# Optimization experiments

Measured on AMD Instinct MI355X. Metric: run time of the kernel, lower is better.

Reference implementation:

```python
import jax, jax.numpy as jnp
import numpy as np

NHEAD = 16
EPS = 1e-5

def layer_norm(x, g, b):
    mu = jnp.mean(x, axis=-1, keepdims=True)
    var = jnp.mean(jnp.square(x - mu), axis=-1, keepdims=True)
    return (x - mu) * jax.lax.rsqrt(var + EPS) * g + b

def setup_inputs() -> dict:
    key = jax.random.key(0)
    ks = jax.random.split(key, 12)
    d_model, d_hid = 1024, 4096  # MHA num_hiddens == dim_feedforward (source quirk)
    B, S = 2, 2048
    s_in = 1.0 / np.sqrt(d_model)
    s_hid = 1.0 / np.sqrt(d_hid)
    return {
        "x": jax.random.normal(ks[0], (B, S, d_model), jnp.float32),
        "Wq": jax.random.normal(ks[1], (d_model, d_hid), jnp.float32) * s_in,
        "Wk": jax.random.normal(ks[2], (d_model, d_hid), jnp.float32) * s_in,
        "Wv": jax.random.normal(ks[3], (d_model, d_hid), jnp.float32) * s_in,
        "Wo": jax.random.normal(ks[4], (d_hid, d_model), jnp.float32) * s_hid,
        "W1": jax.random.normal(ks[5], (d_model, d_hid), jnp.float32) * s_in,
        "b1": jnp.zeros((d_hid,), jnp.float32),
        "W2": jax.random.normal(ks[6], (d_hid, d_model), jnp.float32) * s_hid,
        "b2": jnp.zeros((d_model,), jnp.float32),
        "g1": jnp.ones((d_model,), jnp.float32),
        "be1": jnp.zeros((d_model,), jnp.float32),
        "g2": jnp.ones((d_model,), jnp.float32),
        "be2": jnp.zeros((d_model,), jnp.float32),
    }

def reference(x, Wq, Wk, Wv, Wo, W1, b1, W2, b2, g1, be1, g2, be2):
    B, S, D = x.shape
    H = NHEAD
    # pre-norm attention branch (dropout = identity at eval)
    x1 = layer_norm(x, g1, be1)
    q = (x1 @ Wq).reshape(B, S, H, -1)  # [B,S,H,dh], dh = num_hiddens/H
    k = (x1 @ Wk).reshape(B, S, H, -1)
    v = (x1 @ Wv).reshape(B, S, H, -1)
    dh = q.shape[-1]
    scores = jnp.einsum('bqhd,bkhd->bhqk', q, k) / jnp.sqrt(jnp.float32(dh))
    attn = jax.nn.softmax(scores, axis=-1)
    ctx = jnp.einsum('bhqk,bkhd->bqhd', attn, v).reshape(B, S, -1)
    x = x + ctx @ Wo
    # pre-norm FFN branch
    x2 = layer_norm(x, g2, be2)
    h = jax.nn.relu(x2 @ W1 + b1)
    out = x + (h @ W2 + b2)
    return out
```

## Files before the change

kernel.cpp:

```cpp
#include <hip/hip_runtime.h>
#include <hip/hip_bf16.h>
#include <stdint.h>

using bf16x8 = __attribute__((ext_vector_type(8))) __bf16;
using f32x4  = __attribute__((ext_vector_type(4))) float;

__device__ __forceinline__ uint16_t f2bf(float f) {
    uint32_t u = __builtin_bit_cast(uint32_t, f);
    u += 0x7FFFu + ((u >> 16) & 1u);
    return (uint16_t)(u >> 16);
}
__device__ __forceinline__ uint32_t pack2bf(float lo, float hi) {
    return (uint32_t)f2bf(lo) | ((uint32_t)f2bf(hi) << 16);
}

__device__ __forceinline__ void gld_lds16(const void* g, void* l) {
    __builtin_amdgcn_global_load_lds(
        (const __attribute__((address_space(1))) void*)g,
        (__attribute__((address_space(3))) void*)l,
        16, 0, 0);
}

__global__ __launch_bounds__(256)
void wconv(const float* __restrict__ in, uint16_t* __restrict__ out, int R, int C) {
    __shared__ float t[32][33];
    int c0 = blockIdx.x * 32, r0 = blockIdx.y * 32;
    int tx = threadIdx.x & 31, ty = threadIdx.x >> 5;
    #pragma unroll
    for (int i = 0; i < 32; i += 8)
        t[ty + i][tx] = in[(size_t)(r0 + ty + i) * C + c0 + tx];
    __syncthreads();
    #pragma unroll
    for (int i = 0; i < 32; i += 8)
        out[(size_t)(c0 + ty + i) * R + r0 + tx] = f2bf(t[tx][ty + i]);
}

__global__ __launch_bounds__(256)
void ln_bf16(const float* __restrict__ x, const float* __restrict__ gw,
             const float* __restrict__ bw, uint16_t* __restrict__ out) {
    const int D = 1024;
    int row = blockIdx.x;
    float4 v = ((const float4*)(x + (size_t)row * D))[threadIdx.x];
    float s  = v.x + v.y + v.z + v.w;
    float ss = v.x * v.x + v.y * v.y + v.z * v.z + v.w * v.w;
    #pragma unroll
    for (int m = 1; m < 64; m <<= 1) {
        s  += __shfl_xor(s, m);
        ss += __shfl_xor(ss, m);
    }
    __shared__ float red[8];
    int wid = threadIdx.x >> 6, lane = threadIdx.x & 63;
    if (lane == 0) { red[wid] = s; red[4 + wid] = ss; }
    __syncthreads();
    s  = red[0] + red[1] + red[2] + red[3];
    ss = red[4] + red[5] + red[6] + red[7];
    float mu  = s * (1.f / 1024.f);
    float var = ss * (1.f / 1024.f) - mu * mu;
    float rstd = rsqrtf(var + 1e-5f);
    float4 gv = ((const float4*)gw)[threadIdx.x];
    float4 bv = ((const float4*)bw)[threadIdx.x];
    ushort4 o;
    o.x = f2bf((v.x - mu) * rstd * gv.x + bv.x);
    o.y = f2bf((v.y - mu) * rstd * gv.y + bv.y);
    o.z = f2bf((v.z - mu) * rstd * gv.z + bv.z);
    o.w = f2bf((v.w - mu) * rstd * gv.w + bv.w);
    ((ushort4*)(out + (size_t)row * D))[threadIdx.x] = o;
}

template <int EPI>
__global__ __launch_bounds__(256, 2)
void gemm_bt(const uint16_t* __restrict__ A, const uint16_t* __restrict__ B,
             void* __restrict__ Cp, const float* __restrict__ bias,
             const float* __restrict__ resid, int M, int N, int K) {
    __shared__ uint16_t sA[128 * 32];
    __shared__ uint16_t sB[128 * 32];
    int bid = blockIdx.x;
    int cpx = gridDim.x >> 3;
    bid = (bid & 7) * cpx + (bid >> 3);
    int nbn  = N >> 7;
    int brow = (bid / nbn) << 7;
    int bcol = (bid % nbn) << 7;
    int t = threadIdx.x;
    int wid = t >> 6, lane = t & 63;
    int wr = (wid >> 1) << 6, wc = (wid & 1) << 6;
    int q = lane & 15, g = lane >> 4;

    f32x4 acc[4][4] = {};

    const uint16_t* Abase = A + (size_t)brow * K + ((lane & 3) << 3);
    const uint16_t* Bbase = B + (size_t)bcol * K + ((lane & 3) << 3);
    int rsub = lane >> 2;

    for (int kt = 0; kt < K; kt += 32) {
        __syncthreads();
        #pragma unroll
        for (int i = 0; i < 2; ++i) {
            int chunk = i * 4 + wid;
            int row = chunk * 16 + rsub;
            gld_lds16(Abase + (size_t)row * K + kt, &sA[chunk * 512]);
            gld_lds16(Bbase + (size_t)row * K + kt, &sB[chunk * 512]);
        }
        __syncthreads();
        bf16x8 af[4], bfr[4];
        #pragma unroll
        for (int i = 0; i < 4; ++i)
            af[i] = *(const bf16x8*)&sA[(wr + i * 16 + q) * 32 + g * 8];
        #pragma unroll
        for (int j = 0; j < 4; ++j)
            bfr[j] = *(const bf16x8*)&sB[(wc + j * 16 + q) * 32 + g * 8];
        #pragma unroll
        for (int i = 0; i < 4; ++i)
            #pragma unroll
            for (int j = 0; j < 4; ++j)
                acc[i][j] = __builtin_amdgcn_mfma_f32_16x16x32_bf16(
                    af[i], bfr[j], acc[i][j], 0, 0, 0);
    }

    float* Cf = (float*)Cp;
    #pragma unroll
    for (int i = 0; i < 4; ++i) {
        #pragma unroll
        for (int j = 0; j < 4; ++j) {
            #pragma unroll
            for (int r = 0; r < 4; ++r) {
                int gr = brow + wr + i * 16 + g * 4 + r;
                int gc = bcol + wc + j * 16 + q;
                float v = acc[i][j][r];
                size_t idx = (size_t)gr * N + gc;
                if constexpr (EPI == 2) {
                    Cf[idx] = v + bias[gc] + resid[idx];
                } else {
                    Cf[idx] = v + resid[idx];
                }
            }
        }
    }
}

template <int EPI>
__global__ __launch_bounds__(512, 2)
void gemm256(const uint16_t* __restrict__ A, const uint16_t* __restrict__ B,
             void* __restrict__ Cp, const float* __restrict__ bias,
             int M, int N, int K) {
    __shared__ uint8_t smem[131072];
    int bid = blockIdx.x;
    int cpx = gridDim.x >> 3;
    bid = (bid & 7) * cpx + (bid >> 3);
    int nbn  = N >> 8;
    int brow = (bid / nbn) << 8;
    int bcol = (bid % nbn) << 8;
    int t0 = threadIdx.x;
    int wid = t0 >> 6, lane = t0 & 63;
    int wr = wid >> 2, wc = wid & 3;
    int q = lane & 15, g = lane >> 4;

    const uint16_t* Asw = A + (size_t)(brow + (lane >> 3)) * K + (((lane & 7) ^ (lane >> 3)) << 3);
    const uint16_t* Bsw = B + (size_t)(bcol + (lane >> 3)) * K + (((lane & 7) ^ (lane >> 3)) << 3);

    f32x4 acc[2][2][4][2] = {};
    int NKT = K >> 6;

#define STAGE256(BSEL, KK)                                                     \
    {                                                                          \
        uint8_t* dA = smem + (BSEL) * 32768;                                   \
        uint8_t* dB = smem + 65536 + (BSEL) * 32768;                           \
        _Pragma("unroll")                                                      \
        for (int i = 0; i < 4; ++i) {                                          \
            int c = wid * 4 + i;                                               \
            gld_lds16(Asw + (size_t)(c * 8) * K + (KK), dA + c * 1024);        \
            gld_lds16(Bsw + (size_t)(c * 8) * K + (KK), dB + c * 1024);        \
        }                                                                      \
    }

    STAGE256(0, 0)

    for (int t = 0; t < NKT; ++t) {
        int cur = t & 1;
        if (t + 1 < NKT) {
            STAGE256(cur ^ 1, (t + 1) << 6)
            asm volatile("s_waitcnt vmcnt(8)" ::: "memory");
        } else {
            asm volatile("s_waitcnt vmcnt(0)" ::: "memory");
        }
        __builtin_amdgcn_sched_barrier(0);
        __builtin_amdgcn_s_barrier();
        __builtin_amdgcn_sched_barrier(0);

        const uint8_t* bA = smem + cur * 32768;
        const uint8_t* bB = smem + 65536 + cur * 32768;

        bf16x8 af[4][2], bfr[2][2];

#define LOADA256(MH)                                                           \
        _Pragma("unroll")                                                      \
        for (int m2 = 0; m2 < 4; ++m2)                                         \
            _Pragma("unroll")                                                  \
            for (int ks = 0; ks < 2; ++ks) {                                   \
                int rr = wr * 128 + (MH) * 64 + m2 * 16 + q;                   \
                int sl = (ks * 4 + g) ^ (q & 7);                               \
                af[m2][ks] = *(const bf16x8*)(bA + rr * 128 + sl * 16);        \
            }
#define LOADB256(NH)                                                           \
        _Pragma("unroll")                                                      \
        for (int n2 = 0; n2 < 2; ++n2)                                         \
            _Pragma("unroll")                                                  \
            for (int ks = 0; ks < 2; ++ks) {                                   \
                int cc = wc * 64 + (NH) * 32 + n2 * 16 + q;                    \
                int sl = (ks * 4 + g) ^ (q & 7);                               \
                bfr[n2][ks] = *(const bf16x8*)(bB + cc * 128 + sl * 16);       \
            }
#define MMQ256(MH, NH)                                                         \
        __builtin_amdgcn_s_setprio(1);                                         \
        _Pragma("unroll")                                                      \
        for (int m2 = 0; m2 < 4; ++m2)                                         \
            _Pragma("unroll")                                                  \
            for (int n2 = 0; n2 < 2; ++n2)                                     \
                _Pragma("unroll")                                              \
                for (int ks = 0; ks < 2; ++ks)                                 \
                    acc[MH][NH][m2][n2] = __builtin_amdgcn_mfma_f32_16x16x32_bf16( \
                        af[m2][ks], bfr[n2][ks], acc[MH][NH][m2][n2], 0, 0, 0);\
        __builtin_amdgcn_s_setprio(0);

        LOADA256(0) LOADB256(0) MMQ256(0, 0)
        LOADB256(1) MMQ256(0, 1)
        LOADA256(1) MMQ256(1, 1)
        LOADB256(0) MMQ256(1, 0)

        __builtin_amdgcn_s_barrier();
    }

    uint16_t* Cb = (uint16_t*)Cp;
    #pragma unroll
    for (int mh = 0; mh < 2; ++mh)
        #pragma unroll
        for (int nh = 0; nh < 2; ++nh)
            #pragma unroll
            for (int m2 = 0; m2 < 4; ++m2)
                #pragma unroll
                for (int n2 = 0; n2 < 2; ++n2)
                    #pragma unroll
                    for (int r = 0; r < 4; ++r) {
                        int gr = brow + wr * 128 + mh * 64 + m2 * 16 + g * 4 + r;
                        int gc = bcol + wc * 64 + nh * 32 + n2 * 16 + q;
                        float v = acc[mh][nh][m2][n2][r];
                        if constexpr (EPI == 1) {
                            v += bias[gc];
                            v = v > 0.f ? v : 0.f;
                        }
                        Cb[(size_t)gr * N + gc] = f2bf(v);
                    }
}

__device__ __forceinline__ void attn_stage(uint8_t* smem, int bufsel,
        const uint16_t* Kb0, const uint16_t* Vb0, int ktok, int wid, int lane) {
    #pragma unroll
    for (int i = 0; i < 4; ++i) {
        int chunk = wid * 4 + i;
        int r = 2 * chunk + (lane >> 5);
        int s = lane & 31;
        int cg = (s & ~7) | ((s ^ r) & 7);
        gld_lds16(Kb0 + (size_t)(ktok + r) * 4096 + cg * 8,
                  smem + bufsel * 16384 + chunk * 1024);
    }
    #pragma unroll
    for (int i = 0; i < 4; ++i) {
        int chunk = wid * 4 + i;
        int r = 16 * chunk + (lane >> 2);
        int s = lane & 3;
        int cg = s ^ (r & 3);
        gld_lds16(Vb0 + (size_t)r * 4096 + ktok + cg * 8,
                  smem + 32768 + bufsel * 16384 + chunk * 1024);
    }
}

__device__ __forceinline__ bf16x8 sm_pack(const f32x4* sacc, f32x4* acc,
                                          float& m_run, float& l_run,
                                          int q, int g) {
    float mx = fmaxf(fmaxf(fmaxf(sacc[0][0], sacc[0][1]), fmaxf(sacc[0][2], sacc[0][3])),
                     fmaxf(fmaxf(sacc[1][0], sacc[1][1]), fmaxf(sacc[1][2], sacc[1][3])));
    mx = fmaxf(mx, __shfl_xor(mx, 16));
    mx = fmaxf(mx, __shfl_xor(mx, 32));
    if (!__all(mx - m_run <= 8.f)) {
        float m_new = fmaxf(m_run, mx);
        float alpha = __expf(m_run - m_new);
        l_run *= alpha;
        #pragma unroll
        for (int td = 0; td < 16; ++td) {
            acc[td][0] *= alpha; acc[td][1] *= alpha;
            acc[td][2] *= alpha; acc[td][3] *= alpha;
        }
        m_run = m_new;
    }
    float p[8]; float rs = 0.f;
    #pragma unroll
    for (int tm = 0; tm < 2; ++tm)
        #pragma unroll
        for (int r = 0; r < 4; ++r) {
            float e = __expf(sacc[tm][r] - m_run);
            p[tm * 4 + r] = e; rs += e;
        }
    rs += __shfl_xor(rs, 16);
    rs += __shfl_xor(rs, 32);
    l_run += rs;

    uint32_t pk0 = pack2bf(p[0], p[1]);
    uint32_t pk1 = pack2bf(p[2], p[3]);
    uint32_t pk2 = pack2bf(p[4], p[5]);
    uint32_t pk3 = pack2bf(p[6], p[7]);
    int srcA = ((g & 1) << 5) + q;
    int srcB = srcA + 16;
    uint32_t a0 = __shfl(pk0, srcA), a1 = __shfl(pk2, srcA);
    uint32_t b0 = __shfl(pk1, srcA), b1 = __shfl(pk3, srcA);
    uint32_t c0 = __shfl(pk0, srcB), c1 = __shfl(pk2, srcB);
    uint32_t d0 = __shfl(pk1, srcB), d1 = __shfl(pk3, srcB);
    bool hi = g >= 2;
    uint4 pb;
    pb.x = hi ? a1 : a0;
    pb.y = hi ? b1 : b0;
    pb.z = hi ? c1 : c0;
    pb.w = hi ? d1 : d0;
    return __builtin_bit_cast(bf16x8, pb);
}

__global__ __launch_bounds__(256, 2)
void attn(const uint16_t* __restrict__ Qg, const uint16_t* __restrict__ Kg,
          const uint16_t* __restrict__ Vtg, uint16_t* __restrict__ Og) {
    const int S = 2048, NC = 4096, NT = 64;
    __shared__ uint8_t smem[65536];

    int id = blockIdx.x;
    id = (id & 7) * 64 + (id >> 3);
    int qb = id & 15, h = (id >> 4) & 15, b = id >> 8;

    int t = threadIdx.x;
    int wid = t >> 6, lane = t & 63;
    int q = lane & 15, g = lane >> 4;
    int tok0 = b * S + qb * 128 + wid * 32;

    bf16x8 qf0[8], qf1[8];
    {
        const uint16_t* qrow0 = Qg + (size_t)(tok0 + q) * NC + h * 256 + g * 8;
        const uint16_t* qrow1 = Qg + (size_t)(tok0 + 16 + q) * NC + h * 256 + g * 8;
        #pragma unroll
        for (int c = 0; c < 8; ++c) {
            bf16x8 r0 = *(const bf16x8*)(qrow0 + c * 32);
            bf16x8 r1 = *(const bf16x8*)(qrow1 + c * 32);
            #pragma unroll
            for (int i = 0; i < 8; ++i) {
                r0[i] = (__bf16)((float)r0[i] * 0.0625f);
                r1[i] = (__bf16)((float)r1[i] * 0.0625f);
            }
            qf0[c] = r0; qf1[c] = r1;
        }
    }

    f32x4 acc0[16] = {}, acc1[16] = {};
    float m0 = -1e30f, l0 = 0.f;
    float m1 = -1e30f, l1 = 0.f;

    const uint16_t* Kb0 = Kg + (size_t)(b * S) * NC + h * 256;
    const uint16_t* Vb0 = Vtg + (size_t)(h * 256) * NC + b * S;

    attn_stage(smem, 0, Kb0, Vb0, 0, wid, lane);

    for (int kt = 0; kt < NT; ++kt) {
        int cb = (kt & 1) * 16384;
        if (kt + 1 < NT) {
            attn_stage(smem, (kt + 1) & 1, Kb0, Vb0, (kt + 1) * 32, wid, lane);
            asm volatile("s_waitcnt vmcnt(8)" ::: "memory");
        } else {
            asm volatile("s_waitcnt vmcnt(0)" ::: "memory");
        }
        __builtin_amdgcn_sched_barrier(0);
        __builtin_amdgcn_s_barrier();

        const uint16_t* sk = (const uint16_t*)(smem + cb);
        const uint16_t* sv = (const uint16_t*)(smem + 32768 + cb);

        f32x4 sA0[2] = {}, sA1[2] = {};
        __builtin_amdgcn_s_setprio(1);
        #pragma unroll
        for (int c = 0; c < 8; ++c) {
            #pragma unroll
            for (int tm = 0; tm < 2; ++tm) {
                int G = c * 4 + g;
                int slot = (G & ~7) | ((G ^ q) & 7);
                bf16x8 kf = *(const bf16x8*)(sk + (tm * 16 + q) * 256 + slot * 8);
                sA0[tm] = __builtin_amdgcn_mfma_f32_16x16x32_bf16(kf, qf0[c], sA0[tm], 0, 0, 0);
                sA1[tm] = __builtin_amdgcn_mfma_f32_16x16x32_bf16(kf, qf1[c], sA1[tm], 0, 0, 0);
            }
        }
        __builtin_amdgcn_s_setprio(0);

        bf16x8 pfrag0 = sm_pack(sA0, acc0, m0, l0, q, g);
        bf16x8 pfrag1 = sm_pack(sA1, acc1, m1, l1, q, g);

        int sl = g ^ (q & 3);
        __builtin_amdgcn_s_setprio(1);
        #pragma unroll
        for (int td = 0; td < 16; ++td) {
            bf16x8 vf = *(const bf16x8*)(sv + (td * 16 + q) * 32 + sl * 8);
            acc0[td] = __builtin_amdgcn_mfma_f32_16x16x32_bf16(vf, pfrag0, acc0[td], 0, 0, 0);
            acc1[td] = __builtin_amdgcn_mfma_f32_16x16x32_bf16(vf, pfrag1, acc1[td], 0, 0, 0);
        }
        __builtin_amdgcn_s_setprio(0);
        __builtin_amdgcn_s_barrier();
    }

    __syncthreads();
    {
        float inv0 = 1.f / l0, inv1 = 1.f / l1;
        uint32_t* w0 = (uint32_t*)(smem + wid * 16384);
        uint32_t* w1 = (uint32_t*)(smem + wid * 16384 + 8192);
        #pragma unroll
        for (int td = 0; td < 16; ++td) {
            int base = (q * 256 + td * 16 + g * 4) >> 1;
            w0[base]     = pack2bf(acc0[td][0] * inv0, acc0[td][1] * inv0);
            w0[base + 1] = pack2bf(acc0[td][2] * inv0, acc0[td][3] * inv0);
            w1[base]     = pack2bf(acc1[td][0] * inv1, acc1[td][1] * inv1);
            w1[base + 1] = pack2bf(acc1[td][2] * inv1, acc1[td][3] * inv1);
        }
    }
    __syncthreads();
    #pragma unroll
    for (int s2 = 0; s2 < 2; ++s2) {
        const uint16_t* tb = (const uint16_t*)(smem + wid * 16384 + s2 * 8192);
        #pragma unroll
        for (int r2 = 0; r2 < 8; ++r2) {
            int c = r2 * 64 + lane;
            int qq = c >> 5, dc = c & 31;
            uint4 v = *(const uint4*)&tb[qq * 256 + dc * 8];
            *(uint4*)(Og + (size_t)(tok0 + s2 * 16 + qq) * NC + h * 256 + dc * 8) = v;
        }
    }
}

extern "C" void kernel_launch(void* const* d_in, const int* in_sizes, int n_in,
                              void* d_out, int out_size, void* d_ws, size_t ws_size,
                              hipStream_t stream) {
    const float* x   = (const float*)d_in[0];
    const float* Wq  = (const float*)d_in[1];
    const float* Wk  = (const float*)d_in[2];
    const float* Wv  = (const float*)d_in[3];
    const float* Wo  = (const float*)d_in[4];
    const float* W1  = (const float*)d_in[5];
    const float* b1  = (const float*)d_in[6];
    const float* W2  = (const float*)d_in[7];
    const float* b2  = (const float*)d_in[8];
    const float* g1  = (const float*)d_in[9];
    const float* be1 = (const float*)d_in[10];
    const float* g2  = (const float*)d_in[11];
    const float* be2 = (const float*)d_in[12];

    char* ws = (char*)d_ws;
    const size_t M8 = 8388608;
    uint16_t* WqT  = (uint16_t*)(ws + 0 * M8);
    uint16_t* WkT  = (uint16_t*)(ws + 1 * M8);
    uint16_t* WvT  = (uint16_t*)(ws + 2 * M8);
    uint16_t* WoT  = (uint16_t*)(ws + 3 * M8);
    uint16_t* W1T  = (uint16_t*)(ws + 4 * M8);
    uint16_t* W2T  = (uint16_t*)(ws + 5 * M8);
    uint16_t* x1   = (uint16_t*)(ws + 6 * M8);
    uint16_t* x2   = (uint16_t*)(ws + 7 * M8);
    uint16_t* Q    = (uint16_t*)(ws + 8 * M8);
    uint16_t* Kq   = (uint16_t*)(ws + 12 * M8);
    uint16_t* Vt   = (uint16_t*)(ws + 16 * M8);
    uint16_t* ctx  = (uint16_t*)(ws + 20 * M8);
    float*    xmid = (float*)(ws + 12 * M8);
    uint16_t* Hn   = (uint16_t*)(ws + 8 * M8);

    wconv<<<dim3(128, 32), 256, 0, stream>>>(Wq, WqT, 1024, 4096);
    wconv<<<dim3(128, 32), 256, 0, stream>>>(Wk, WkT, 1024, 4096);
    wconv<<<dim3(128, 32), 256, 0, stream>>>(Wv, WvT, 1024, 4096);
    wconv<<<dim3(32, 128), 256, 0, stream>>>(Wo, WoT, 4096, 1024);
    wconv<<<dim3(128, 32), 256, 0, stream>>>(W1, W1T, 1024, 4096);
    wconv<<<dim3(32, 128), 256, 0, stream>>>(W2, W2T, 4096, 1024);

    ln_bf16<<<4096, 256, 0, stream>>>(x, g1, be1, x1);

    gemm256<0><<<256, 512, 0, stream>>>(x1, WqT, Q,  nullptr, 4096, 4096, 1024);
    gemm256<0><<<256, 512, 0, stream>>>(x1, WkT, Kq, nullptr, 4096, 4096, 1024);
    gemm256<0><<<256, 512, 0, stream>>>(WvT, x1, Vt, nullptr, 4096, 4096, 1024);

    attn<<<512, 256, 0, stream>>>(Q, Kq, Vt, ctx);

    gemm_bt<3><<<256, 256, 0, stream>>>(ctx, WoT, xmid, nullptr, x, 4096, 1024, 4096);

    ln_bf16<<<4096, 256, 0, stream>>>(xmid, g2, be2, x2);

    gemm256<1><<<256, 512, 0, stream>>>(x2, W1T, Hn, b1, 4096, 4096, 1024);
    gemm_bt<2><<<256, 256, 0, stream>>>(Hn, W2T, d_out, b2, xmid, 4096, 1024, 4096);
}
```

Baseline: 520.5 us.

## Shrink gemm256 tile to 256x128 with triple-buffered LDS prefetch

The big-GEMM kernel moves from a 256x256 output tile to 256x128, doubling the grid to 512 blocks, and replaces the double buffer with a three-stage LDS ring that prefetches two K-steps ahead. Fragment loads and MFMA blocks are split into two halves separated by barriers. The goal is to fill more CUs (256 blocks on 256 CUs left no slack) and to hide global-load latency better. The cost is one block per CU at 144KB LDS, more B-operand reloads per output, and extra barriers per iteration.

```diff
diff --git a/kernel.cpp b/kernel.cpp
--- a/kernel.cpp
+++ b/kernel.cpp
@@ -138,17 +138,17 @@
 }
 
 template <int EPI>
-__global__ __launch_bounds__(512, 2)
+__global__ __launch_bounds__(512, 1)
 void gemm256(const uint16_t* __restrict__ A, const uint16_t* __restrict__ B,
              void* __restrict__ Cp, const float* __restrict__ bias,
              int M, int N, int K) {
-    __shared__ uint8_t smem[131072];
+    __shared__ uint8_t smem[147456];
     int bid = blockIdx.x;
     int cpx = gridDim.x >> 3;
     bid = (bid & 7) * cpx + (bid >> 3);
-    int nbn  = N >> 8;
+    int nbn  = N >> 7;
     int brow = (bid / nbn) << 8;
-    int bcol = (bid % nbn) << 8;
+    int bcol = (bid % nbn) << 7;
     int t0 = threadIdx.x;
     int wid = t0 >> 6, lane = t0 & 63;
     int wr = wid >> 2, wc = wid & 3;
@@ -157,98 +157,123 @@
     const uint16_t* Asw = A + (size_t)(brow + (lane >> 3)) * K + (((lane & 7) ^ (lane >> 3)) << 3);
     const uint16_t* Bsw = B + (size_t)(bcol + (lane >> 3)) * K + (((lane & 7) ^ (lane >> 3)) << 3);
 
-    f32x4 acc[2][2][4][2] = {};
+    f32x4 acc[8][2] = {};
     int NKT = K >> 6;
 
-#define STAGE256(BSEL, KK)                                                     \
+#define STG(BUF, KK)                                                           \
     {                                                                          \
-        uint8_t* dA = smem + (BSEL) * 32768;                                   \
-        uint8_t* dB = smem + 65536 + (BSEL) * 32768;                           \
+        uint8_t* dA = smem + (BUF) * 49152;                                    \
+        uint8_t* dB = dA + 32768;                                              \
         _Pragma("unroll")                                                      \
         for (int i = 0; i < 4; ++i) {                                          \
             int c = wid * 4 + i;                                               \
             gld_lds16(Asw + (size_t)(c * 8) * K + (KK), dA + c * 1024);        \
+        }                                                                      \
+        _Pragma("unroll")                                                      \
+        for (int i = 0; i < 2; ++i) {                                          \
+            int c = wid * 2 + i;                                               \
             gld_lds16(Bsw + (size_t)(c * 8) * K + (KK), dB + c * 1024);        \
         }                                                                      \
     }
 
-    STAGE256(0, 0)
-
+    STG(0, 0)
+    STG(1, 64)
+
+    int cur = 0;
     for (int t = 0; t < NKT; ++t) {
-        int cur = t & 1;
-        if (t + 1 < NKT) {
-            STAGE256(cur ^ 1, (t + 1) << 6)
-            asm volatile("s_waitcnt vmcnt(8)" ::: "memory");
+        int nxt2 = cur + 2; if (nxt2 >= 3) nxt2 -= 3;
+        if (t + 2 < NKT) {
+            STG(nxt2, (t + 2) << 6)
+            asm volatile("s_waitcnt vmcnt(12)" ::: "memory");
+        } else if (t + 1 < NKT) {
+            asm volatile("s_waitcnt vmcnt(6)" ::: "memory");
         } else {
             asm volatile("s_waitcnt vmcnt(0)" ::: "memory");
         }
         __builtin_amdgcn_sched_barrier(0);
         __builtin_amdgcn_s_barrier();
+
+        const uint8_t* bA = smem + cur * 49152;
+        const uint8_t* bB = bA + 32768;
+
+        bf16x8 af[4][2], bfr[2][2];
+
+        #pragma unroll
+        for (int m2 = 0; m2 < 4; ++m2)
+            #pragma unroll
+            for (int ks = 0; ks < 2; ++ks) {
+                int rr = wr * 128 + m2 * 16 + q;
+                int sl = (ks * 4 + g) ^ (q & 7);
+                af[m2][ks] = *(const bf16x8*)(bA + rr * 128 + sl * 16);
+            }
+        #pragma unroll
+        for (int n2 = 0; n2 < 2; ++n2)
+            #pragma unroll
+            for (int ks = 0; ks < 2; ++ks) {
+                int cc = wc * 32 + n2 * 16 + q;
+                int sl = (ks * 4 + g) ^ (q & 7);
+                bfr[n2][ks] = *(const bf16x8*)(bB + cc * 128 + sl * 16);
+            }
         __builtin_amdgcn_sched_barrier(0);
-
-        const uint8_t* bA = smem + cur * 32768;
-        const uint8_t* bB = smem + 65536 + cur * 32768;
-
-        bf16x8 af[4][2], bfr[2][2];
-
-#define LOADA256(MH)                                                           \
-        _Pragma("unroll")                                                      \
-        for (int m2 = 0; m2 < 4; ++m2)                                         \
-            _Pragma("unroll")                                                  \
-            for (int ks = 0; ks < 2; ++ks) {                                   \
-                int rr = wr * 128 + (MH) * 64 + m2 * 16 + q;                   \
-                int sl = (ks * 4 + g) ^ (q & 7);                               \
-                af[m2][ks] = *(const bf16x8*)(bA + rr * 128 + sl * 16);        \
-            }
-#define LOADB256(NH)                                                           \
-        _Pragma("unroll")                                                      \
-        for (int n2 = 0; n2 < 2; ++n2)                                         \
-            _Pragma("unroll")                                                  \
-            for (int ks = 0; ks < 2; ++ks) {                                   \
-                int cc = wc * 64 + (NH) * 32 + n2 * 16 + q;                    \
-                int sl = (ks * 4 + g) ^ (q & 7);                               \
-                bfr[n2][ks] = *(const bf16x8*)(bB + cc * 128 + sl * 16);       \
-            }
-#define MMQ256(MH, NH)                                                         \
-        __builtin_amdgcn_s_setprio(1);                                         \
-        _Pragma("unroll")                                                      \
-        for (int m2 = 0; m2 < 4; ++m2)                                         \
-            _Pragma("unroll")                                                  \
-            for (int n2 = 0; n2 < 2; ++n2)                                     \
-                _Pragma("unroll")                                              \
-                for (int ks = 0; ks < 2; ++ks)                                 \
-                    acc[MH][NH][m2][n2] = __builtin_amdgcn_mfma_f32_16x16x32_bf16( \
-                        af[m2][ks], bfr[n2][ks], acc[MH][NH][m2][n2], 0, 0, 0);\
+        __builtin_amdgcn_s_barrier();
+        asm volatile("s_waitcnt lgkmcnt(0)" ::: "memory");
+        __builtin_amdgcn_sched_barrier(0);
+        __builtin_amdgcn_s_setprio(1);
+        #pragma unroll
+        for (int m2 = 0; m2 < 4; ++m2)
+            #pragma unroll
+            for (int n2 = 0; n2 < 2; ++n2)
+                #pragma unroll
+                for (int ks = 0; ks < 2; ++ks)
+                    acc[m2][n2] = __builtin_amdgcn_mfma_f32_16x16x32_bf16(
+                        af[m2][ks], bfr[n2][ks], acc[m2][n2], 0, 0, 0);
         __builtin_amdgcn_s_setprio(0);
-
-        LOADA256(0) LOADB256(0) MMQ256(0, 0)
-        LOADB256(1) MMQ256(0, 1)
-        LOADA256(1) MMQ256(1, 1)
-        LOADB256(0) MMQ256(1, 0)
-
-        __builtin_amdgcn_s_barrier();
+        __builtin_amdgcn_s_barrier();
+
+        #pragma unroll
+        for (int m2 = 0; m2 < 4; ++m2)
+            #pragma unroll
+            for (int ks = 0; ks < 2; ++ks) {
+                int rr = wr * 128 + 64 + m2 * 16 + q;
+                int sl = (ks * 4 + g) ^ (q & 7);
+                af[m2][ks] = *(const bf16x8*)(bA + rr * 128 + sl * 16);
+            }
+        __builtin_amdgcn_sched_barrier(0);
+        __builtin_amdgcn_s_barrier();
+        asm volatile("s_waitcnt lgkmcnt(0)" ::: "memory");
+        __builtin_amdgcn_sched_barrier(0);
+        __builtin_amdgcn_s_setprio(1);
+        #pragma unroll
+        for (int m2 = 0; m2 < 4; ++m2)
+            #pragma unroll
+            for (int n2 = 0; n2 < 2; ++n2)
+                #pragma unroll
+                for (int ks = 0; ks < 2; ++ks)
+                    acc[4 + m2][n2] = __builtin_amdgcn_mfma_f32_16x16x32_bf16(
+                        af[m2][ks], bfr[n2][ks], acc[4 + m2][n2], 0, 0, 0);
+        __builtin_amdgcn_s_setprio(0);
+        __builtin_amdgcn_s_barrier();
+
+        cur = cur + 1; if (cur >= 3) cur -= 3;
     }
 
     uint16_t* Cb = (uint16_t*)Cp;
     #pragma unroll
-    for (int mh = 0; mh < 2; ++mh)
-        #pragma unroll
-        for (int nh = 0; nh < 2; ++nh)
-            #pragma unroll
-            for (int m2 = 0; m2 < 4; ++m2)
-                #pragma unroll
-                for (int n2 = 0; n2 < 2; ++n2)
-                    #pragma unroll
-                    for (int r = 0; r < 4; ++r) {
-                        int gr = brow + wr * 128 + mh * 64 + m2 * 16 + g * 4 + r;
-                        int gc = bcol + wc * 64 + nh * 32 + n2 * 16 + q;
-                        float v = acc[mh][nh][m2][n2][r];
-                        if constexpr (EPI == 1) {
-                            v += bias[gc];
-                            v = v > 0.f ? v : 0.f;
-                        }
-                        Cb[(size_t)gr * N + gc] = f2bf(v);
-                    }
+    for (int m2 = 0; m2 < 8; ++m2)
+        #pragma unroll
+        for (int n2 = 0; n2 < 2; ++n2)
+            #pragma unroll
+            for (int r = 0; r < 4; ++r) {
+                int gr = brow + wr * 128 + (m2 >> 2) * 64 + (m2 & 3) * 16 + g * 4 + r;
+                int gc = bcol + wc * 32 + n2 * 16 + q;
+                float v = acc[m2][n2][r];
+                if constexpr (EPI == 1) {
+                    v += bias[gc];
+                    v = v > 0.f ? v : 0.f;
+                }
+                Cb[(size_t)gr * N + gc] = f2bf(v);
+            }
+#undef STG
 }
 
 __device__ __forceinline__ void attn_stage(uint8_t* smem, int bufsel,
@@ -478,9 +503,9 @@
 
     ln_bf16<<<4096, 256, 0, stream>>>(x, g1, be1, x1);
 
-    gemm256<0><<<256, 512, 0, stream>>>(x1, WqT, Q,  nullptr, 4096, 4096, 1024);
-    gemm256<0><<<256, 512, 0, stream>>>(x1, WkT, Kq, nullptr, 4096, 4096, 1024);
-    gemm256<0><<<256, 512, 0, stream>>>(WvT, x1, Vt, nullptr, 4096, 4096, 1024);
+    gemm256<0><<<512, 512, 0, stream>>>(x1, WqT, Q,  nullptr, 4096, 4096, 1024);
+    gemm256<0><<<512, 512, 0, stream>>>(x1, WkT, Kq, nullptr, 4096, 4096, 1024);
+    gemm256<0><<<512, 512, 0, stream>>>(WvT, x1, Vt, nullptr, 4096, 4096, 1024);
 
     attn<<<512, 256, 0, stream>>>(Q, Kq, Vt, ctx);
 
@@ -488,6 +513,6 @@
 
     ln_bf16<<<4096, 256, 0, stream>>>(xmid, g2, be2, x2);
 
-    gemm256<1><<<256, 512, 0, stream>>>(x2, W1T, Hn, b1, 4096, 4096, 1024);
+    gemm256<1><<<512, 512, 0, stream>>>(x2, W1T, Hn, b1, 4096, 4096, 1024);
     gemm_bt<2><<<256, 256, 0, stream>>>(Hn, W2T, d_out, b2, xmid, 4096, 1024, 4096);
 }
```

Measured after the change: 566.3 us. 1.09x slower.

## Fuse Q and K projections into one GEMM and split attention K/V waits

Applied to the files above, without the earlier changes.

WqT and WkT sit next to each other in the workspace, so the Q and K projections run as one GEMM with N=8192, writing an interleaved QK buffer with row stride 8192. The attention kernel reads Q and K at that stride. The idea is to cut a launch and get better occupancy from 512 blocks. Attention now waits only for the K tile before the QK^T MFMAs, and waits for V with a second barrier after the softmax, so V loads overlap compute. The cost is an extra barrier per iteration and strided QK reads.

```diff
diff --git a/kernel.cpp b/kernel.cpp
--- a/kernel.cpp
+++ b/kernel.cpp
@@ -249,6 +249,10 @@
                         }
                         Cb[(size_t)gr * N + gc] = f2bf(v);
                     }
+#undef STAGE256
+#undef LOADA256
+#undef LOADB256
+#undef MMQ256
 }
 
 __device__ __forceinline__ void attn_stage(uint8_t* smem, int bufsel,
@@ -259,7 +263,7 @@
         int r = 2 * chunk + (lane >> 5);
         int s = lane & 31;
         int cg = (s & ~7) | ((s ^ r) & 7);
-        gld_lds16(Kb0 + (size_t)(ktok + r) * 4096 + cg * 8,
+        gld_lds16(Kb0 + (size_t)(ktok + r) * 8192 + cg * 8,
                   smem + bufsel * 16384 + chunk * 1024);
     }
     #pragma unroll
@@ -325,7 +329,7 @@
 __global__ __launch_bounds__(256, 2)
 void attn(const uint16_t* __restrict__ Qg, const uint16_t* __restrict__ Kg,
           const uint16_t* __restrict__ Vtg, uint16_t* __restrict__ Og) {
-    const int S = 2048, NC = 4096, NT = 64;
+    const int S = 2048, NT = 64, QKS = 8192, OC = 4096;
     __shared__ uint8_t smem[65536];
 
     int id = blockIdx.x;
@@ -339,8 +343,8 @@
 
     bf16x8 qf0[8], qf1[8];
     {
-        const uint16_t* qrow0 = Qg + (size_t)(tok0 + q) * NC + h * 256 + g * 8;
-        const uint16_t* qrow1 = Qg + (size_t)(tok0 + 16 + q) * NC + h * 256 + g * 8;
+        const uint16_t* qrow0 = Qg + (size_t)(tok0 + q) * QKS + h * 256 + g * 8;
+        const uint16_t* qrow1 = Qg + (size_t)(tok0 + 16 + q) * QKS + h * 256 + g * 8;
         #pragma unroll
         for (int c = 0; c < 8; ++c) {
             bf16x8 r0 = *(const bf16x8*)(qrow0 + c * 32);
@@ -358,8 +362,8 @@
     float m0 = -1e30f, l0 = 0.f;
     float m1 = -1e30f, l1 = 0.f;
 
-    const uint16_t* Kb0 = Kg + (size_t)(b * S) * NC + h * 256;
-    const uint16_t* Vb0 = Vtg + (size_t)(h * 256) * NC + b * S;
+    const uint16_t* Kb0 = Kg + (size_t)(b * S) * QKS + h * 256;
+    const uint16_t* Vb0 = Vtg + (size_t)(h * 256) * 4096 + b * S;
 
     attn_stage(smem, 0, Kb0, Vb0, 0, wid, lane);
 
@@ -367,9 +371,9 @@
         int cb = (kt & 1) * 16384;
         if (kt + 1 < NT) {
             attn_stage(smem, (kt + 1) & 1, Kb0, Vb0, (kt + 1) * 32, wid, lane);
-            asm volatile("s_waitcnt vmcnt(8)" ::: "memory");
+            asm volatile("s_waitcnt vmcnt(12)" ::: "memory");
         } else {
-            asm volatile("s_waitcnt vmcnt(0)" ::: "memory");
+            asm volatile("s_waitcnt vmcnt(4)" ::: "memory");
         }
         __builtin_amdgcn_sched_barrier(0);
         __builtin_amdgcn_s_barrier();
@@ -395,6 +399,14 @@
         bf16x8 pfrag0 = sm_pack(sA0, acc0, m0, l0, q, g);
         bf16x8 pfrag1 = sm_pack(sA1, acc1, m1, l1, q, g);
 
+        if (kt + 1 < NT) {
+            asm volatile("s_waitcnt vmcnt(8)" ::: "memory");
+        } else {
+            asm volatile("s_waitcnt vmcnt(0)" ::: "memory");
+        }
+        __builtin_amdgcn_sched_barrier(0);
+        __builtin_amdgcn_s_barrier();
+
         int sl = g ^ (q & 3);
         __builtin_amdgcn_s_setprio(1);
         #pragma unroll
@@ -430,7 +442,7 @@
             int c = r2 * 64 + lane;
             int qq = c >> 5, dc = c & 31;
             uint4 v = *(const uint4*)&tb[qq * 256 + dc * 8];
-            *(uint4*)(Og + (size_t)(tok0 + s2 * 16 + qq) * NC + h * 256 + dc * 8) = v;
+            *(uint4*)(Og + (size_t)(tok0 + s2 * 16 + qq) * OC + h * 256 + dc * 8) = v;
         }
     }
 }
@@ -454,7 +466,8 @@
 
     char* ws = (char*)d_ws;
     const size_t M8 = 8388608;
-    uint16_t* WqT  = (uint16_t*)(ws + 0 * M8);
+    uint16_t* WqkT = (uint16_t*)(ws + 0 * M8);
+    uint16_t* WqT  = WqkT;
     uint16_t* WkT  = (uint16_t*)(ws + 1 * M8);
     uint16_t* WvT  = (uint16_t*)(ws + 2 * M8);
     uint16_t* WoT  = (uint16_t*)(ws + 3 * M8);
@@ -462,8 +475,7 @@
     uint16_t* W2T  = (uint16_t*)(ws + 5 * M8);
     uint16_t* x1   = (uint16_t*)(ws + 6 * M8);
     uint16_t* x2   = (uint16_t*)(ws + 7 * M8);
-    uint16_t* Q    = (uint16_t*)(ws + 8 * M8);
-    uint16_t* Kq   = (uint16_t*)(ws + 12 * M8);
+    uint16_t* QK   = (uint16_t*)(ws + 8 * M8);
     uint16_t* Vt   = (uint16_t*)(ws + 16 * M8);
     uint16_t* ctx  = (uint16_t*)(ws + 20 * M8);
     float*    xmid = (float*)(ws + 12 * M8);
@@ -478,11 +490,10 @@
 
     ln_bf16<<<4096, 256, 0, stream>>>(x, g1, be1, x1);
 
-    gemm256<0><<<256, 512, 0, stream>>>(x1, WqT, Q,  nullptr, 4096, 4096, 1024);
-    gemm256<0><<<256, 512, 0, stream>>>(x1, WkT, Kq, nullptr, 4096, 4096, 1024);
+    gemm256<0><<<512, 512, 0, stream>>>(x1, WqkT, QK, nullptr, 4096, 8192, 1024);
     gemm256<0><<<256, 512, 0, stream>>>(WvT, x1, Vt, nullptr, 4096, 4096, 1024);
 
-    attn<<<512, 256, 0, stream>>>(Q, Kq, Vt, ctx);
+    attn<<<512, 256, 0, stream>>>(QK, QK + 4096, Vt, ctx);
 
     gemm_bt<3><<<256, 256, 0, stream>>>(ctx, WoT, xmid, nullptr, x, 4096, 1024, 4096);
 
```

New measurement: 524.9 us. About the same (+0.9%).
